# Kernel optimization log

Measured on AMD Instinct MI355X. Metric: run time of the kernel, lower is better.

## Reference

```python
import jax, jax.numpy as jnp
import numpy as np

B, E, T, H = 2, 1024, 2048, 16
DH = E // H


def _conv1x1(x, W, b, mask):
    # x: [B,C,T], W: [O,C], b: [O], mask: [B,1,T] (norm=False -> plain conv on masked input)
    x = x * mask
    return jnp.einsum('oc,bct->bot', W, x) + b[None, :, None]


def setup_inputs() -> dict:
    key = jax.random.key(0)
    ks = jax.random.split(key, 16)
    inp = {
        'q': jax.random.normal(ks[0], (B, E, T), jnp.float32),
        'k': jax.random.normal(ks[1], (B, E, T), jnp.float32),
        'v': jax.random.normal(ks[2], (B, E, T), jnp.float32),
        'query_mask': (jax.random.uniform(ks[3], (B, 1, T)) < 0.9).astype(jnp.float32),
        'key_mask': (jax.random.uniform(ks[4], (B, 1, T)) < 0.9).astype(jnp.float32),
        'value_mask': (jax.random.uniform(ks[5], (B, 1, T)) < 0.9).astype(jnp.float32),
        'Wq': jax.random.normal(ks[6], (E, E), jnp.float32) * (1.0 / np.sqrt(E)),
        'bq': jnp.zeros((E,), jnp.float32),
        'Wk': jax.random.normal(ks[7], (E, E), jnp.float32) * (1.0 / np.sqrt(E)),
        'bk': jnp.zeros((E,), jnp.float32),
        'Wv': jax.random.normal(ks[8], (E, E), jnp.float32) * (1.0 / np.sqrt(E)),
        'bv': jnp.zeros((E,), jnp.float32),
        'Wo': jax.random.normal(ks[9], (E, E), jnp.float32) * (1.0 / np.sqrt(E)),
        'bo': jnp.zeros((E,), jnp.float32),
    }
    return inp


def reference(q, k, v, query_mask, key_mask, value_mask, Wq, bq, Wk, bk, Wv, bv, Wo, bo):
    # 1x1 conv projections with input masking (norm=False path)
    qp = _conv1x1(q, Wq, bq, query_mask)   # [B,E,T]
    kp = _conv1x1(k, Wk, bk, key_mask)
    vp = _conv1x1(v, Wv, bv, value_mask)
    # split heads: [B,E,T] -> [B,H,DH,T]
    qh = qp.reshape(B, H, DH, T)
    kh = kp.reshape(B, H, DH, T)
    vh = vp.reshape(B, H, DH, T)
    # scores = q^T k with pre-softmax multiplicative masks, scaled by sqrt(embed_dim)
    scores = jnp.einsum('bhdq,bhdk->bhqk', qh, kh)
    scores = scores * query_mask[:, :, :, None] * key_mask[:, :, None, :] / np.sqrt(E)
    attn = jax.nn.softmax(scores, axis=-1) * key_mask[:, :, None, :]  # post-softmax mask
    # transpose_scores=False path: v @ scores (contracts v's time dim with the query dim)
    out = jnp.einsum('bhdq,bhqk->bhdk', vh, attn)  # [B,H,DH,T]
    out = out.reshape(B, E, T)
    return _conv1x1(out, Wo, bo, key_mask)
```

## Files before the change

### kernel.cpp

```cpp
#include <hip/hip_runtime.h>

#define B 2
#define E 1024
#define T 2048
#define H 16
#define DH 64

#define SCALE2 0.0450842200277801f

typedef _Float16 f16x8 __attribute__((ext_vector_type(8)));
typedef float f32x4 __attribute__((ext_vector_type(4)));
typedef float f32x16 __attribute__((ext_vector_type(16)));
typedef unsigned short ushort8v __attribute__((ext_vector_type(8)));
typedef unsigned int uint4v __attribute__((ext_vector_type(4)));

__device__ __forceinline__ f32x4 mfma16(f16x8 a, f16x8 b, f32x4 c) {
  return __builtin_amdgcn_mfma_f32_16x16x32_f16(a, b, c, 0, 0, 0);
}
__device__ __forceinline__ f32x16 mfma32(f16x8 a, f16x8 b, f32x16 c) {
  return __builtin_amdgcn_mfma_f32_32x32x16_f16(a, b, c, 0, 0, 0);
}
__device__ __forceinline__ unsigned short f16u(float x) {
  _Float16 h = (_Float16)x;
  return __builtin_bit_cast(unsigned short, h);
}
__device__ __forceinline__ float ex2(float x) {
  return __builtin_amdgcn_exp2f(x);
}
__device__ __forceinline__ unsigned int pk16(float a, float b) {
  auto h = __builtin_amdgcn_cvt_pkrtz(a, b);
  return __builtin_bit_cast(unsigned int, h);
}
__device__ __forceinline__ void plswap(unsigned int& a, unsigned int& b) {
  auto r = __builtin_amdgcn_permlane32_swap(a, b, false, false);
  a = r[0];
  b = r[1];
}

__global__ __launch_bounds__(256) void prep_weights(
    const float* __restrict__ Wq, const float* __restrict__ Wk,
    const float* __restrict__ Wv, const float* __restrict__ Wo,
    unsigned short* __restrict__ WqB, unsigned short* __restrict__ WkB,
    unsigned short* __restrict__ WvB, unsigned short* __restrict__ WoB) {
  const int which = blockIdx.y;
  const int i = (blockIdx.x * 256 + threadIdx.x) * 4;
  const float* src = which == 0 ? Wq : which == 1 ? Wk : which == 2 ? Wv : Wo;
  unsigned short* dst = which == 0 ? WqB : which == 1 ? WkB : which == 2 ? WvB : WoB;
  float4 v = *(const float4*)&src[i];
  ((unsigned int*)&dst[i])[0] = f16u(v.x) | ((unsigned)f16u(v.y) << 16);
  ((unsigned int*)&dst[i])[1] = f16u(v.z) | ((unsigned)f16u(v.w) << 16);
}

__global__ __launch_bounds__(256) void transpose_cvt(
    const float* __restrict__ q, const float* __restrict__ k,
    const float* __restrict__ v, unsigned short* __restrict__ XtQ,
    unsigned short* __restrict__ XtK, unsigned short* __restrict__ XtV) {
  __shared__ float Xs[32 * 36];
  const int z = blockIdx.z, which = z >> 1, b = z & 1;
  const float* X = which == 0 ? q : which == 1 ? k : v;
  unsigned short* O = which == 0 ? XtQ : which == 1 ? XtK : XtV;
  const int e0 = blockIdx.y * 32, t0 = blockIdx.x * 32;
  const int tid = threadIdx.x;
  const int r = tid >> 3, c = (tid & 7) * 4;
  *(float4*)&Xs[r * 36 + c] = *(const float4*)&X[((size_t)b * E + e0 + r) * T + t0 + c];
  __syncthreads();
  unsigned short h[4];
#pragma unroll
  for (int j = 0; j < 4; ++j) h[j] = f16u(Xs[(c + j) * 36 + r]);
  const size_t o = ((size_t)b * T + t0 + r) * E + e0 + c;
  ((unsigned int*)&O[o])[0] = h[0] | ((unsigned)h[1] << 16);
  ((unsigned int*)&O[o])[1] = h[2] | ((unsigned)h[3] << 16);
}

__global__ __launch_bounds__(256) void proj_qkv(
    const unsigned short* __restrict__ WqB, const unsigned short* __restrict__ WkB,
    const unsigned short* __restrict__ WvB, const unsigned short* __restrict__ XtQ,
    const unsigned short* __restrict__ XtK, const unsigned short* __restrict__ XtV,
    const float* __restrict__ bq, const float* __restrict__ bk,
    const float* __restrict__ bv, const float* __restrict__ qmask,
    const float* __restrict__ kmask, const float* __restrict__ vmask,
    unsigned short* __restrict__ qp2, unsigned short* __restrict__ kp2,
    unsigned short* __restrict__ vp) {
  __shared__ unsigned short Ah[128 * 72], Bs[128 * 72];
  const int b = blockIdx.z, my = blockIdx.y;
  const int which = my >> 3, o0 = (my & 7) * 128, t0 = blockIdx.x * 128;
  const unsigned short* W = which == 0 ? WqB : which == 1 ? WkB : WvB;
  const unsigned short* Xt = which == 0 ? XtQ : which == 1 ? XtK : XtV;
  const float* bias = which == 0 ? bq : which == 1 ? bk : bv;
  const float* mask = which == 0 ? qmask : which == 1 ? kmask : vmask;

  const int tid = threadIdx.x, wave = tid >> 6, lane = tid & 63;
  const int lg = lane & 15, quad = lane >> 4;
  const int wm = (wave & 1) * 64, wn = (wave >> 1) * 64;
  const int sr = tid >> 3, sc = (tid & 7) * 8;

  f32x4 acc[4][4];
#pragma unroll
  for (int i = 0; i < 4; ++i)
#pragma unroll
    for (int j = 0; j < 4; ++j) acc[i][j] = (f32x4){0.f, 0.f, 0.f, 0.f};

  for (int k0 = 0; k0 < E; k0 += 64) {
    ushort8v ra[4], rb[4];
#pragma unroll
    for (int p = 0; p < 4; ++p) {
      ra[p] = *(const ushort8v*)&W[(size_t)(o0 + p * 32 + sr) * E + k0 + sc];
      rb[p] = *(const ushort8v*)&Xt[((size_t)b * T + t0 + p * 32 + sr) * E + k0 + sc];
    }
    __syncthreads();
#pragma unroll
    for (int p = 0; p < 4; ++p) {
      *(ushort8v*)&Ah[(p * 32 + sr) * 72 + sc] = ra[p];
      *(ushort8v*)&Bs[(p * 32 + sr) * 72 + sc] = rb[p];
    }
    __syncthreads();
    f16x8 af[4][2];
#pragma unroll
    for (int mt = 0; mt < 4; ++mt) {
      af[mt][0] = *(const f16x8*)&Ah[(wm + mt * 16 + lg) * 72 + quad * 8];
      af[mt][1] = *(const f16x8*)&Ah[(wm + mt * 16 + lg) * 72 + 32 + quad * 8];
    }
#pragma unroll
    for (int nt = 0; nt < 4; ++nt) {
      f16x8 b0 = *(const f16x8*)&Bs[(wn + nt * 16 + lg) * 72 + quad * 8];
      f16x8 b1 = *(const f16x8*)&Bs[(wn + nt * 16 + lg) * 72 + 32 + quad * 8];
#pragma unroll
      for (int mt = 0; mt < 4; ++mt) {
        f32x4 c = acc[mt][nt];
        c = mfma16(af[mt][0], b0, c);
        c = mfma16(af[mt][1], b1, c);
        acc[mt][nt] = c;
      }
    }
  }
#pragma unroll
  for (int nt = 0; nt < 4; ++nt) {
    const int tcol = t0 + wn + nt * 16 + lg;
    const float mv = mask[b * T + tcol];
#pragma unroll
    for (int mt = 0; mt < 4; ++mt) {
      const int oF = o0 + wm + mt * 16 + quad * 4;
      float v4[4];
      if (which == 0) {
        const float s = mv * SCALE2;
#pragma unroll
        for (int r = 0; r < 4; ++r) v4[r] = (acc[mt][nt][r] + bias[oF + r]) * s;
      } else if (which == 1) {
#pragma unroll
        for (int r = 0; r < 4; ++r) v4[r] = (acc[mt][nt][r] + bias[oF + r]) * mv;
      } else {
#pragma unroll
        for (int r = 0; r < 4; ++r) v4[r] = acc[mt][nt][r] * mv + bias[oF + r];
      }
      if (which <= 1) {
        unsigned short* O = which == 0 ? qp2 : kp2;
        const int head = (o0 + wm) >> 6;
        const int bh2 = b * H + head;
        const size_t idx8 =
            (((size_t)(bh2 * (T / 32) + (tcol >> 5)) * 4 + mt) * 32 + (tcol & 31)) * 2 +
            (quad >> 1);
        unsigned int* dst = (unsigned int*)(O + idx8 * 8 + (quad & 1) * 4);
        dst[0] = f16u(v4[0]) | ((unsigned)f16u(v4[1]) << 16);
        dst[1] = f16u(v4[2]) | ((unsigned)f16u(v4[3]) << 16);
      } else {
#pragma unroll
        for (int r = 0; r < 4; ++r)
          vp[((size_t)b * E + oF + r) * T + tcol] = f16u(v4[r]);
      }
    }
  }
}

__global__ __launch_bounds__(256) void repack_v(
    const unsigned short* __restrict__ vp, unsigned short* __restrict__ vp2) {
  __shared__ unsigned short Ls[64 * 136];
  const int q0 = blockIdx.x * 128, hh = blockIdx.y, b = blockIdx.z;
  const int bh = b * H + hh;
  const int tid = threadIdx.x;
#pragma unroll
  for (int w = 0; w < 2; ++w) {
    const int d = w * 32 + (tid >> 3);
    const int c = (tid & 7) * 16;
    const unsigned short* src = vp + ((size_t)b * E + hh * DH + d) * T + q0 + c;
    *(ushort8v*)&Ls[d * 136 + c] = *(const ushort8v*)src;
    *(ushort8v*)&Ls[d * 136 + c + 8] = *(const ushort8v*)(src + 8);
  }
  __syncthreads();
#pragma unroll
  for (int w = 0; w < 4; ++w) {
    const int flat = w * 256 + tid;
    const int hb = flat & 1, lnv = (flat >> 1) & 31, dt = (flat >> 6) & 1,
              qgl = flat >> 7;
    ushort8v val = *(const ushort8v*)&Ls[(dt * 32 + lnv) * 136 + qgl * 16 + hb * 8];
    const size_t idx8 =
        (((size_t)(bh * (T / 16) + (q0 >> 4) + qgl) * 2 + dt) * 32 + lnv) * 2 + hb;
    *(ushort8v*)&vp2[idx8 * 8] = val;
  }
}

__global__ __launch_bounds__(256) void attn_stats(
    const unsigned short* __restrict__ qp2, const unsigned short* __restrict__ kp2,
    float* __restrict__ sPart) {
  const int bh = blockIdx.y;
  const int z = blockIdx.z;
  const int q0 = blockIdx.x * 128;
  const int tid = threadIdx.x, wave = tid >> 6, lane = tid & 63;
  const int ln = lane & 31, half = lane >> 5;

  const int t32q = (q0 >> 5) + wave;
  f16x8 aq[4];
#pragma unroll
  for (int s = 0; s < 4; ++s)
    aq[s] = *(const f16x8*)&qp2[((((size_t)bh * (T / 32) + t32q) * 4 + s) * 64 +
                                 ln * 2 + half) * 8];

  float lacc[16];
#pragma unroll
  for (int r = 0; r < 16; ++r) lacc[r] = 0.f;

  const int kbase = z * (T / 2);
  const int kend = kbase + T / 2;

  f16x8 bkr[2][4];
#pragma unroll
  for (int nt = 0; nt < 2; ++nt)
#pragma unroll
    for (int s = 0; s < 4; ++s)
      bkr[nt][s] = *(const f16x8*)&kp2[((((size_t)bh * (T / 32) + (kbase >> 5) + nt) * 4 +
                                         s) * 64 + ln * 2 + half) * 8];

  for (int kt = kbase; kt < kend; kt += 64) {
    const int kn = (kt + 64 < kend) ? kt + 64 : kbase;
    f16x8 nb[2][4];
#pragma unroll
    for (int nt = 0; nt < 2; ++nt)
#pragma unroll
      for (int s = 0; s < 4; ++s)
        nb[nt][s] =
            *(const f16x8*)&kp2[((((size_t)bh * (T / 32) + (kn >> 5) + nt) * 4 + s) * 64 +
                                 ln * 2 + half) * 8];
    f32x16 S0 = {}, S1 = {};
#pragma unroll
    for (int s = 0; s < 4; ++s) {
      S0 = mfma32(aq[s], bkr[0][s], S0);
      S1 = mfma32(aq[s], bkr[1][s], S1);
    }
#pragma unroll
    for (int r = 0; r < 16; ++r) lacc[r] += ex2(S0[r]) + ex2(S1[r]);
#pragma unroll
    for (int nt = 0; nt < 2; ++nt)
#pragma unroll
      for (int s = 0; s < 4; ++s) bkr[nt][s] = nb[nt][s];
  }
#pragma unroll
  for (int off = 1; off < 32; off <<= 1)
#pragma unroll
    for (int r = 0; r < 16; ++r) lacc[r] += __shfl_xor(lacc[r], off, 64);
  if (ln == 0) {
#pragma unroll
    for (int t = 0; t < 4; ++t) {
      f32x4 o;
#pragma unroll
      for (int j = 0; j < 4; ++j) o[j] = lacc[t * 4 + j];
      *(f32x4*)&sPart[((size_t)z * (B * H) + bh) * T + q0 + wave * 32 + t * 8 +
                      half * 4] = o;
    }
  }
}

__global__ __launch_bounds__(256) void stats_merge(
    const float* __restrict__ sPart, float* __restrict__ lLog) {
  const int i = (blockIdx.x * 256 + threadIdx.x) * 4;
  const int N = B * H * T;
  f32x4 a = *(const f32x4*)&sPart[i];
  f32x4 b = *(const f32x4*)&sPart[N + i];
  f32x4 o;
#pragma unroll
  for (int j = 0; j < 4; ++j) o[j] = -__builtin_amdgcn_logf(a[j] + b[j]);
  *(f32x4*)&lLog[i] = o;
}

__global__ __launch_bounds__(256) void attn_apply(
    const unsigned short* __restrict__ qp2, const unsigned short* __restrict__ kp2,
    const unsigned short* __restrict__ vp2, const float* __restrict__ lLog,
    float* __restrict__ aPart) {
  __shared__ float st[32 * 130];
  const int bh = blockIdx.y;
  const int z = blockIdx.z;
  const int kblk = blockIdx.x * 64;
  const int tid = threadIdx.x, wave = tid >> 6, lane = tid & 63;
  const int ln = lane & 31, half = lane >> 5;
  const int kt = wave & 1, qh = wave >> 1;

  const int t32k = (kblk >> 5) + kt;
  f16x8 bkk[4];
#pragma unroll
  for (int s = 0; s < 4; ++s)
    bkk[s] = *(const f16x8*)&kp2[((((size_t)bh * (T / 32) + t32k) * 4 + s) * 64 +
                                  ln * 2 + half) * 8];

  f32x16 acc0 = {}, acc1 = {};
  const int qstart = (z * 2 + qh) * (T / 4);
  const int qend = qstart + T / 4;

  f16x8 aqN[4], avN[2][2];
  f32x4 llN[4];
#pragma unroll
  for (int s = 0; s < 4; ++s)
    aqN[s] = *(const f16x8*)&qp2[((((size_t)bh * (T / 32) + (qstart >> 5)) * 4 + s) * 64 +
                                  ln * 2 + half) * 8];
#pragma unroll
  for (int dt = 0; dt < 2; ++dt)
#pragma unroll
    for (int f = 0; f < 2; ++f)
      avN[dt][f] = *(const f16x8*)&vp2[((((size_t)bh * (T / 16) + (qstart >> 4) + f) * 2 +
                                         dt) * 32 + ln) * 16 + half * 8];
#pragma unroll
  for (int t = 0; t < 4; ++t)
    llN[t] = *(const f32x4*)&lLog[(size_t)bh * T + qstart + t * 8 + half * 4];

  for (int qt = qstart; qt < qend; qt += 32) {
    f16x8 aq[4], av[2][2];
    f32x4 ll[4];
#pragma unroll
    for (int s = 0; s < 4; ++s) aq[s] = aqN[s];
#pragma unroll
    for (int dt = 0; dt < 2; ++dt)
#pragma unroll
      for (int f = 0; f < 2; ++f) av[dt][f] = avN[dt][f];
#pragma unroll
    for (int t = 0; t < 4; ++t) ll[t] = llN[t];
    const int qn = qt + 32 < qend ? qt + 32 : qstart;
#pragma unroll
    for (int s = 0; s < 4; ++s)
      aqN[s] = *(const f16x8*)&qp2[((((size_t)bh * (T / 32) + (qn >> 5)) * 4 + s) * 64 +
                                    ln * 2 + half) * 8];
#pragma unroll
    for (int dt = 0; dt < 2; ++dt)
#pragma unroll
      for (int f = 0; f < 2; ++f)
        avN[dt][f] = *(const f16x8*)&vp2[((((size_t)bh * (T / 16) + (qn >> 4) + f) * 2 +
                                           dt) * 32 + ln) * 16 + half * 8];
#pragma unroll
    for (int t = 0; t < 4; ++t)
      llN[t] = *(const f32x4*)&lLog[(size_t)bh * T + qn + t * 8 + half * 4];
    f32x16 S = {};
#pragma unroll
    for (int s = 0; s < 4; ++s) S = mfma32(aq[s], bkk[s], S);
    unsigned int w[8];
#pragma unroll
    for (int p = 0; p < 8; ++p) {
      const float e0 = ex2(S[p * 2 + 0] + ll[p >> 1][(p & 1) * 2 + 0]);
      const float e1 = ex2(S[p * 2 + 1] + ll[p >> 1][(p & 1) * 2 + 1]);
      w[p] = pk16(e0, e1);
    }
    plswap(w[0], w[2]);
    plswap(w[1], w[3]);
    plswap(w[4], w[6]);
    plswap(w[5], w[7]);
    uint4v f0, f1;
    f0[0] = w[0]; f0[1] = w[1]; f0[2] = w[2]; f0[3] = w[3];
    f1[0] = w[4]; f1[1] = w[5]; f1[2] = w[6]; f1[3] = w[7];
    const f16x8 pf0 = __builtin_bit_cast(f16x8, f0);
    const f16x8 pf1 = __builtin_bit_cast(f16x8, f1);
    acc0 = mfma32(av[0][0], pf0, acc0);
    acc0 = mfma32(av[0][1], pf1, acc0);
    acc1 = mfma32(av[1][0], pf0, acc1);
    acc1 = mfma32(av[1][1], pf1, acc1);
  }

  __syncthreads();
  if (qh == 1) {
#pragma unroll
    for (int i = 0; i < 16; ++i) {
      st[i * 130 + kt * 65 + lane] = acc0[i];
      st[(16 + i) * 130 + kt * 65 + lane] = acc1[i];
    }
  }
  __syncthreads();
  if (qh == 0) {
#pragma unroll
    for (int i = 0; i < 16; ++i) {
      acc0[i] += st[i * 130 + kt * 65 + lane];
      acc1[i] += st[(16 + i) * 130 + kt * 65 + lane];
    }
    const int kcol = kblk + kt * 32 + ln;
    float* dst = aPart + ((size_t)(z * B * H + bh) * T + kcol) * DH;
#pragma unroll
    for (int dt = 0; dt < 2; ++dt) {
      const float* a = dt ? (const float*)&acc1 : (const float*)&acc0;
#pragma unroll
      for (int t = 0; t < 4; ++t) {
        f32x4 o;
#pragma unroll
        for (int j = 0; j < 4; ++j) o[j] = a[t * 4 + j];
        *(f32x4*)&dst[dt * 32 + t * 8 + half * 4] = o;
      }
    }
  }
}

__global__ __launch_bounds__(256) void apply_merge(
    const float* __restrict__ aPart, unsigned short* __restrict__ ao) {
  const size_t i = ((size_t)blockIdx.x * 256 + threadIdx.x) * 8;
  const size_t NZ = (size_t)B * H * T * DH;
  f32x4 a0 = *(const f32x4*)&aPart[i];
  f32x4 a1 = *(const f32x4*)&aPart[i + 4];
  f32x4 b0 = *(const f32x4*)&aPart[NZ + i];
  f32x4 b1 = *(const f32x4*)&aPart[NZ + i + 4];
  unsigned short h[8];
#pragma unroll
  for (int j = 0; j < 4; ++j) h[j] = f16u(a0[j] + b0[j]);
#pragma unroll
  for (int j = 0; j < 4; ++j) h[4 + j] = f16u(a1[j] + b1[j]);
  const int bh = (int)(i >> 17);
  const int rem = (int)(i & (T * DH - 1));
  const int k = rem >> 6, d = rem & 63;
  uint4v u;
  u[0] = h[0] | ((unsigned)h[1] << 16);
  u[1] = h[2] | ((unsigned)h[3] << 16);
  u[2] = h[4] | ((unsigned)h[5] << 16);
  u[3] = h[6] | ((unsigned)h[7] << 16);
  *(uint4v*)&ao[((size_t)(bh >> 4) * T + k) * E + (bh & 15) * 64 + d] = u;
}

__global__ __launch_bounds__(256) void proj_final(
    const unsigned short* __restrict__ WoB, const unsigned short* __restrict__ ao,
    const float* __restrict__ bo, const float* __restrict__ kmask,
    float* __restrict__ out) {
  __shared__ unsigned short As[64 * 68], Bs[128 * 68];
  const int b = blockIdx.z, o0 = blockIdx.y * 64, t0 = blockIdx.x * 128;
  const int tid = threadIdx.x, wave = tid >> 6, lane = tid & 63;
  const int ln = lane & 31, half = lane >> 5;
  const int wn = wave * 32;
  const int ar = tid >> 2, ac = (tid & 3) * 16;
  const int br = tid >> 1, bc = (tid & 1) * 32;

  f32x16 acc0 = {}, acc1 = {};

  for (int k0 = 0; k0 < E; k0 += 64) {
    ushort8v a0 = *(const ushort8v*)&WoB[(size_t)(o0 + ar) * E + k0 + ac];
    ushort8v a1 = *(const ushort8v*)&WoB[(size_t)(o0 + ar) * E + k0 + ac + 8];
    ushort8v b0 = *(const ushort8v*)&ao[((size_t)b * T + t0 + br) * E + k0 + bc];
    ushort8v b1 = *(const ushort8v*)&ao[((size_t)b * T + t0 + br) * E + k0 + bc + 8];
    ushort8v b2 = *(const ushort8v*)&ao[((size_t)b * T + t0 + br) * E + k0 + bc + 16];
    ushort8v b3 = *(const ushort8v*)&ao[((size_t)b * T + t0 + br) * E + k0 + bc + 24];
    __syncthreads();
    *(ushort8v*)&As[ar * 68 + ac] = a0;
    *(ushort8v*)&As[ar * 68 + ac + 8] = a1;
    *(ushort8v*)&Bs[br * 68 + bc] = b0;
    *(ushort8v*)&Bs[br * 68 + bc + 8] = b1;
    *(ushort8v*)&Bs[br * 68 + bc + 16] = b2;
    *(ushort8v*)&Bs[br * 68 + bc + 24] = b3;
    __syncthreads();
#pragma unroll
    for (int s = 0; s < 4; ++s) {
      f16x8 af0 = *(const f16x8*)&As[ln * 68 + s * 16 + half * 8];
      f16x8 af1 = *(const f16x8*)&As[(32 + ln) * 68 + s * 16 + half * 8];
      f16x8 bf = *(const f16x8*)&Bs[(wn + ln) * 68 + s * 16 + half * 8];
      acc0 = mfma32(af0, bf, acc0);
      acc1 = mfma32(af1, bf, acc1);
    }
  }
  const int tcol = t0 + wn + ln;
  const float mv = kmask[b * T + tcol];
#pragma unroll
  for (int dt = 0; dt < 2; ++dt) {
    const float* a = dt ? (const float*)&acc1 : (const float*)&acc0;
#pragma unroll
    for (int t = 0; t < 4; ++t)
#pragma unroll
      for (int j = 0; j < 4; ++j) {
        const int e = o0 + dt * 32 + t * 8 + half * 4 + j;
        out[((size_t)b * E + e) * T + tcol] = a[t * 4 + j] * mv + bo[e];
      }
  }
}

extern "C" void kernel_launch(void* const* d_in, const int* in_sizes, int n_in,
                              void* d_out, int out_size, void* d_ws, size_t ws_size,
                              hipStream_t stream) {
  const float* q = (const float*)d_in[0];
  const float* k = (const float*)d_in[1];
  const float* v = (const float*)d_in[2];
  const float* qmask = (const float*)d_in[3];
  const float* kmask = (const float*)d_in[4];
  const float* vmask = (const float*)d_in[5];
  const float* Wq = (const float*)d_in[6];
  const float* bq = (const float*)d_in[7];
  const float* Wk = (const float*)d_in[8];
  const float* bk = (const float*)d_in[9];
  const float* Wv = (const float*)d_in[10];
  const float* bv = (const float*)d_in[11];
  const float* Wo = (const float*)d_in[12];
  const float* bo = (const float*)d_in[13];

  char* w = (char*)d_ws;
  const size_t WB = (size_t)E * E * sizeof(unsigned short);
  const size_t TB = (size_t)B * T * E * sizeof(unsigned short);
  unsigned short* WqB = (unsigned short*)(w + 0 * WB);
  unsigned short* WkB = (unsigned short*)(w + 1 * WB);
  unsigned short* WvB = (unsigned short*)(w + 2 * WB);
  unsigned short* WoB = (unsigned short*)(w + 3 * WB);
  size_t off = 4 * WB;
  unsigned short* XtQ = (unsigned short*)(w + off); off += TB;
  unsigned short* qp2 = (unsigned short*)(w + off); off += TB;
  unsigned short* kp2 = (unsigned short*)(w + off); off += TB;
  unsigned short* vp2 = (unsigned short*)(w + off); off += TB;
  float* lLog = (float*)(w + off); off += (size_t)B * H * T * sizeof(float);
  float* sPart = (float*)(w + off); off += (size_t)2 * B * H * T * sizeof(float);
  unsigned short* XtK = (unsigned short*)(w + off); off += TB;
  unsigned short* XtV = (unsigned short*)(w + off); off += TB;
  unsigned short* vp  = (unsigned short*)(w + off); off += TB;
  float* aPart = (float*)XtK;
  unsigned short* ao = XtQ;

  dim3 bl(256);
  prep_weights<<<dim3((E * E) / 1024, 4), bl, 0, stream>>>(
      Wq, Wk, Wv, Wo, WqB, WkB, WvB, WoB);
  transpose_cvt<<<dim3(T / 32, E / 32, 3 * B), bl, 0, stream>>>(
      q, k, v, XtQ, XtK, XtV);
  proj_qkv<<<dim3(T / 128, 24, B), bl, 0, stream>>>(
      WqB, WkB, WvB, XtQ, XtK, XtV, bq, bk, bv, qmask, kmask, vmask, qp2, kp2, vp);
  repack_v<<<dim3(T / 128, H, B), bl, 0, stream>>>(vp, vp2);
  attn_stats<<<dim3(T / 128, B * H, 2), bl, 0, stream>>>(qp2, kp2, sPart);
  stats_merge<<<dim3((B * H * T) / 1024), bl, 0, stream>>>(sPart, lLog);
  attn_apply<<<dim3(T / 64, B * H, 2), bl, 0, stream>>>(qp2, kp2, vp2, lLog, aPart);
  apply_merge<<<dim3((B * H * T * DH) / 2048), bl, 0, stream>>>(aPart, ao);
  proj_final<<<dim3(T / 128, E / 64, B), bl, 0, stream>>>(
      WoB, ao, bo, kmask, (float*)d_out);
}
```

Before: 282.1 us.

## Enlarge attention tiles, drop apply split-Q partials and fuse merge into attn_apply

attn_stats now gives each wave two 32-row query tiles, so every loaded K fragment is reused across twice as many queries. attn_apply covers 128 keys per block (64 per wave) over half the query range instead of splitting queries across grid z. This removes the fp32 aPart partial buffer and the apply_merge kernel, and the kernel writes fp16 output directly in the ao layout. The cost is more registers (four accumulators plus two score tiles), half as many blocks, and a longer serial loop per wave.

```diff
diff --git a/kernel.cpp b/kernel.cpp
--- a/kernel.cpp
+++ b/kernel.cpp
@@ -203,20 +203,22 @@
     float* __restrict__ sPart) {
   const int bh = blockIdx.y;
   const int z = blockIdx.z;
-  const int q0 = blockIdx.x * 128;
+  const int q0 = blockIdx.x * 256;
   const int tid = threadIdx.x, wave = tid >> 6, lane = tid & 63;
   const int ln = lane & 31, half = lane >> 5;
 
-  const int t32q = (q0 >> 5) + wave;
-  f16x8 aq[4];
-#pragma unroll
-  for (int s = 0; s < 4; ++s)
-    aq[s] = *(const f16x8*)&qp2[((((size_t)bh * (T / 32) + t32q) * 4 + s) * 64 +
-                                 ln * 2 + half) * 8];
-
-  float lacc[16];
-#pragma unroll
-  for (int r = 0; r < 16; ++r) lacc[r] = 0.f;
+  const int t32q = (q0 >> 5) + wave * 2;
+  f16x8 aq[2][4];
+#pragma unroll
+  for (int qs = 0; qs < 2; ++qs)
+#pragma unroll
+    for (int s = 0; s < 4; ++s)
+      aq[qs][s] = *(const f16x8*)&qp2[((((size_t)bh * (T / 32) + t32q + qs) * 4 + s) * 64 +
+                                       ln * 2 + half) * 8];
+
+  float lacc[32];
+#pragma unroll
+  for (int r = 0; r < 32; ++r) lacc[r] = 0.f;
 
   const int kbase = z * (T / 2);
   const int kend = kbase + T / 2;
@@ -239,14 +241,17 @@
         nb[nt][s] =
             *(const f16x8*)&kp2[((((size_t)bh * (T / 32) + (kn >> 5) + nt) * 4 + s) * 64 +
                                  ln * 2 + half) * 8];
-    f32x16 S0 = {}, S1 = {};
-#pragma unroll
-    for (int s = 0; s < 4; ++s) {
-      S0 = mfma32(aq[s], bkr[0][s], S0);
-      S1 = mfma32(aq[s], bkr[1][s], S1);
-    }
-#pragma unroll
-    for (int r = 0; r < 16; ++r) lacc[r] += ex2(S0[r]) + ex2(S1[r]);
+#pragma unroll
+    for (int qs = 0; qs < 2; ++qs) {
+      f32x16 S0 = {}, S1 = {};
+#pragma unroll
+      for (int s = 0; s < 4; ++s) {
+        S0 = mfma32(aq[qs][s], bkr[0][s], S0);
+        S1 = mfma32(aq[qs][s], bkr[1][s], S1);
+      }
+#pragma unroll
+      for (int r = 0; r < 16; ++r) lacc[qs * 16 + r] += ex2(S0[r]) + ex2(S1[r]);
+    }
 #pragma unroll
     for (int nt = 0; nt < 2; ++nt)
 #pragma unroll
@@ -255,16 +260,18 @@
 #pragma unroll
   for (int off = 1; off < 32; off <<= 1)
 #pragma unroll
-    for (int r = 0; r < 16; ++r) lacc[r] += __shfl_xor(lacc[r], off, 64);
+    for (int r = 0; r < 32; ++r) lacc[r] += __shfl_xor(lacc[r], off, 64);
   if (ln == 0) {
 #pragma unroll
-    for (int t = 0; t < 4; ++t) {
-      f32x4 o;
-#pragma unroll
-      for (int j = 0; j < 4; ++j) o[j] = lacc[t * 4 + j];
-      *(f32x4*)&sPart[((size_t)z * (B * H) + bh) * T + q0 + wave * 32 + t * 8 +
-                      half * 4] = o;
-    }
+    for (int qs = 0; qs < 2; ++qs)
+#pragma unroll
+      for (int t = 0; t < 4; ++t) {
+        f32x4 o;
+#pragma unroll
+        for (int j = 0; j < 4; ++j) o[j] = lacc[qs * 16 + t * 4 + j];
+        *(f32x4*)&sPart[((size_t)z * (B * H) + bh) * T + q0 + wave * 64 + qs * 32 +
+                        t * 8 + half * 4] = o;
+      }
   }
 }
 
@@ -283,28 +290,28 @@
 __global__ __launch_bounds__(256) void attn_apply(
     const unsigned short* __restrict__ qp2, const unsigned short* __restrict__ kp2,
     const unsigned short* __restrict__ vp2, const float* __restrict__ lLog,
-    float* __restrict__ aPart) {
-  __shared__ float st[32 * 130];
-  const int bh = blockIdx.y;
-  const int z = blockIdx.z;
-  const int kblk = blockIdx.x * 64;
+    unsigned short* __restrict__ ao) {
+  __shared__ float st[64 * 130];
+  const int bh = blockIdx.y, b = bh >> 4, h = bh & 15;
+  const int kblk = blockIdx.x * 128;
   const int tid = threadIdx.x, wave = tid >> 6, lane = tid & 63;
   const int ln = lane & 31, half = lane >> 5;
   const int kt = wave & 1, qh = wave >> 1;
 
-  const int t32k = (kblk >> 5) + kt;
-  f16x8 bkk[4];
-#pragma unroll
-  for (int s = 0; s < 4; ++s)
-    bkk[s] = *(const f16x8*)&kp2[((((size_t)bh * (T / 32) + t32k) * 4 + s) * 64 +
-                                  ln * 2 + half) * 8];
-
-  f32x16 acc0 = {}, acc1 = {};
-  const int qstart = (z * 2 + qh) * (T / 4);
-  const int qend = qstart + T / 4;
+  const int t32k = (kblk >> 5) + kt * 2;
+  f16x8 bkk[2][4];
+#pragma unroll
+  for (int sub = 0; sub < 2; ++sub)
+#pragma unroll
+    for (int s = 0; s < 4; ++s)
+      bkk[sub][s] = *(const f16x8*)&kp2[((((size_t)bh * (T / 32) + t32k + sub) * 4 + s) *
+                                             64 + ln * 2 + half) * 8];
+
+  f32x16 acc00 = {}, acc01 = {}, acc10 = {}, acc11 = {};
+  const int qstart = qh * (T / 2);
+  const int qend = qstart + T / 2;
 
   f16x8 aqN[4], avN[2][2];
-  f32x4 llN[4];
 #pragma unroll
   for (int s = 0; s < 4; ++s)
     aqN[s] = *(const f16x8*)&qp2[((((size_t)bh * (T / 32) + (qstart >> 5)) * 4 + s) * 64 +
@@ -315,21 +322,15 @@
     for (int f = 0; f < 2; ++f)
       avN[dt][f] = *(const f16x8*)&vp2[((((size_t)bh * (T / 16) + (qstart >> 4) + f) * 2 +
                                          dt) * 32 + ln) * 16 + half * 8];
-#pragma unroll
-  for (int t = 0; t < 4; ++t)
-    llN[t] = *(const f32x4*)&lLog[(size_t)bh * T + qstart + t * 8 + half * 4];
 
   for (int qt = qstart; qt < qend; qt += 32) {
     f16x8 aq[4], av[2][2];
-    f32x4 ll[4];
 #pragma unroll
     for (int s = 0; s < 4; ++s) aq[s] = aqN[s];
 #pragma unroll
     for (int dt = 0; dt < 2; ++dt)
 #pragma unroll
       for (int f = 0; f < 2; ++f) av[dt][f] = avN[dt][f];
-#pragma unroll
-    for (int t = 0; t < 4; ++t) ll[t] = llN[t];
     const int qn = qt + 32 < qend ? qt + 32 : qstart;
 #pragma unroll
     for (int s = 0; s < 4; ++s)
@@ -341,87 +342,98 @@
       for (int f = 0; f < 2; ++f)
         avN[dt][f] = *(const f16x8*)&vp2[((((size_t)bh * (T / 16) + (qn >> 4) + f) * 2 +
                                            dt) * 32 + ln) * 16 + half * 8];
+    f32x4 ll[4];
 #pragma unroll
     for (int t = 0; t < 4; ++t)
-      llN[t] = *(const f32x4*)&lLog[(size_t)bh * T + qn + t * 8 + half * 4];
-    f32x16 S = {};
-#pragma unroll
-    for (int s = 0; s < 4; ++s) S = mfma32(aq[s], bkk[s], S);
-    unsigned int w[8];
-#pragma unroll
-    for (int p = 0; p < 8; ++p) {
-      const float e0 = ex2(S[p * 2 + 0] + ll[p >> 1][(p & 1) * 2 + 0]);
-      const float e1 = ex2(S[p * 2 + 1] + ll[p >> 1][(p & 1) * 2 + 1]);
-      w[p] = pk16(e0, e1);
-    }
-    plswap(w[0], w[2]);
-    plswap(w[1], w[3]);
-    plswap(w[4], w[6]);
-    plswap(w[5], w[7]);
-    uint4v f0, f1;
-    f0[0] = w[0]; f0[1] = w[1]; f0[2] = w[2]; f0[3] = w[3];
-    f1[0] = w[4]; f1[1] = w[5]; f1[2] = w[6]; f1[3] = w[7];
-    const f16x8 pf0 = __builtin_bit_cast(f16x8, f0);
-    const f16x8 pf1 = __builtin_bit_cast(f16x8, f1);
-    acc0 = mfma32(av[0][0], pf0, acc0);
-    acc0 = mfma32(av[0][1], pf1, acc0);
-    acc1 = mfma32(av[1][0], pf0, acc1);
-    acc1 = mfma32(av[1][1], pf1, acc1);
+      ll[t] = *(const f32x4*)&lLog[(size_t)bh * T + qt + t * 8 + half * 4];
+    f32x16 S0 = {}, S1 = {};
+#pragma unroll
+    for (int s = 0; s < 4; ++s) S0 = mfma32(aq[s], bkk[0][s], S0);
+#pragma unroll
+    for (int s = 0; s < 4; ++s) S1 = mfma32(aq[s], bkk[1][s], S1);
+    {
+      unsigned int w[8];
+#pragma unroll
+      for (int p = 0; p < 8; ++p) {
+        const float e0 = ex2(S0[p * 2 + 0] + ll[p >> 1][(p & 1) * 2 + 0]);
+        const float e1 = ex2(S0[p * 2 + 1] + ll[p >> 1][(p & 1) * 2 + 1]);
+        w[p] = pk16(e0, e1);
+      }
+      plswap(w[0], w[2]);
+      plswap(w[1], w[3]);
+      plswap(w[4], w[6]);
+      plswap(w[5], w[7]);
+      uint4v f0v, f1v;
+      f0v[0] = w[0]; f0v[1] = w[1]; f0v[2] = w[2]; f0v[3] = w[3];
+      f1v[0] = w[4]; f1v[1] = w[5]; f1v[2] = w[6]; f1v[3] = w[7];
+      const f16x8 pf0 = __builtin_bit_cast(f16x8, f0v);
+      const f16x8 pf1 = __builtin_bit_cast(f16x8, f1v);
+      acc00 = mfma32(av[0][0], pf0, acc00);
+      acc00 = mfma32(av[0][1], pf1, acc00);
+      acc01 = mfma32(av[1][0], pf0, acc01);
+      acc01 = mfma32(av[1][1], pf1, acc01);
+    }
+    {
+      unsigned int w[8];
+#pragma unroll
+      for (int p = 0; p < 8; ++p) {
+        const float e0 = ex2(S1[p * 2 + 0] + ll[p >> 1][(p & 1) * 2 + 0]);
+        const float e1 = ex2(S1[p * 2 + 1] + ll[p >> 1][(p & 1) * 2 + 1]);
+        w[p] = pk16(e0, e1);
+      }
+      plswap(w[0], w[2]);
+      plswap(w[1], w[3]);
+      plswap(w[4], w[6]);
+      plswap(w[5], w[7]);
+      uint4v f0v, f1v;
+      f0v[0] = w[0]; f0v[1] = w[1]; f0v[2] = w[2]; f0v[3] = w[3];
+      f1v[0] = w[4]; f1v[1] = w[5]; f1v[2] = w[6]; f1v[3] = w[7];
+      const f16x8 pf0 = __builtin_bit_cast(f16x8, f0v);
+      const f16x8 pf1 = __builtin_bit_cast(f16x8, f1v);
+      acc10 = mfma32(av[0][0], pf0, acc10);
+      acc10 = mfma32(av[0][1], pf1, acc10);
+      acc11 = mfma32(av[1][0], pf0, acc11);
+      acc11 = mfma32(av[1][1], pf1, acc11);
+    }
   }
 
   __syncthreads();
   if (qh == 1) {
 #pragma unroll
     for (int i = 0; i < 16; ++i) {
-      st[i * 130 + kt * 65 + lane] = acc0[i];
-      st[(16 + i) * 130 + kt * 65 + lane] = acc1[i];
+      st[(0 * 16 + i) * 130 + kt * 65 + lane] = acc00[i];
+      st[(1 * 16 + i) * 130 + kt * 65 + lane] = acc01[i];
+      st[(2 * 16 + i) * 130 + kt * 65 + lane] = acc10[i];
+      st[(3 * 16 + i) * 130 + kt * 65 + lane] = acc11[i];
     }
   }
   __syncthreads();
   if (qh == 0) {
 #pragma unroll
     for (int i = 0; i < 16; ++i) {
-      acc0[i] += st[i * 130 + kt * 65 + lane];
-      acc1[i] += st[(16 + i) * 130 + kt * 65 + lane];
-    }
-    const int kcol = kblk + kt * 32 + ln;
-    float* dst = aPart + ((size_t)(z * B * H + bh) * T + kcol) * DH;
-#pragma unroll
-    for (int dt = 0; dt < 2; ++dt) {
-      const float* a = dt ? (const float*)&acc1 : (const float*)&acc0;
-#pragma unroll
-      for (int t = 0; t < 4; ++t) {
-        f32x4 o;
-#pragma unroll
-        for (int j = 0; j < 4; ++j) o[j] = a[t * 4 + j];
-        *(f32x4*)&dst[dt * 32 + t * 8 + half * 4] = o;
-      }
-    }
-  }
-}
-
-__global__ __launch_bounds__(256) void apply_merge(
-    const float* __restrict__ aPart, unsigned short* __restrict__ ao) {
-  const size_t i = ((size_t)blockIdx.x * 256 + threadIdx.x) * 8;
-  const size_t NZ = (size_t)B * H * T * DH;
-  f32x4 a0 = *(const f32x4*)&aPart[i];
-  f32x4 a1 = *(const f32x4*)&aPart[i + 4];
-  f32x4 b0 = *(const f32x4*)&aPart[NZ + i];
-  f32x4 b1 = *(const f32x4*)&aPart[NZ + i + 4];
-  unsigned short h[8];
-#pragma unroll
-  for (int j = 0; j < 4; ++j) h[j] = f16u(a0[j] + b0[j]);
-#pragma unroll
-  for (int j = 0; j < 4; ++j) h[4 + j] = f16u(a1[j] + b1[j]);
-  const int bh = (int)(i >> 17);
-  const int rem = (int)(i & (T * DH - 1));
-  const int k = rem >> 6, d = rem & 63;
-  uint4v u;
-  u[0] = h[0] | ((unsigned)h[1] << 16);
-  u[1] = h[2] | ((unsigned)h[3] << 16);
-  u[2] = h[4] | ((unsigned)h[5] << 16);
-  u[3] = h[6] | ((unsigned)h[7] << 16);
-  *(uint4v*)&ao[((size_t)(bh >> 4) * T + k) * E + (bh & 15) * 64 + d] = u;
+      acc00[i] += st[(0 * 16 + i) * 130 + kt * 65 + lane];
+      acc01[i] += st[(1 * 16 + i) * 130 + kt * 65 + lane];
+      acc10[i] += st[(2 * 16 + i) * 130 + kt * 65 + lane];
+      acc11[i] += st[(3 * 16 + i) * 130 + kt * 65 + lane];
+    }
+#pragma unroll
+    for (int sub = 0; sub < 2; ++sub) {
+      const int kcol = kblk + kt * 64 + sub * 32 + ln;
+      const size_t obase = ((size_t)b * T + kcol) * E + h * DH;
+#pragma unroll
+      for (int dt = 0; dt < 2; ++dt) {
+        const float* a = sub == 0 ? (dt ? (const float*)&acc01 : (const float*)&acc00)
+                                  : (dt ? (const float*)&acc11 : (const float*)&acc10);
+#pragma unroll
+        for (int t = 0; t < 4; ++t) {
+          uint2 wv;
+          wv.x = f16u(a[t * 4 + 0]) | ((unsigned)f16u(a[t * 4 + 1]) << 16);
+          wv.y = f16u(a[t * 4 + 2]) | ((unsigned)f16u(a[t * 4 + 3]) << 16);
+          *(uint2*)&ao[obase + dt * 32 + t * 8 + half * 4] = wv;
+        }
+      }
+    }
+  }
 }
 
 __global__ __launch_bounds__(256) void proj_final(
@@ -512,7 +524,6 @@
   unsigned short* XtK = (unsigned short*)(w + off); off += TB;
   unsigned short* XtV = (unsigned short*)(w + off); off += TB;
   unsigned short* vp  = (unsigned short*)(w + off); off += TB;
-  float* aPart = (float*)XtK;
   unsigned short* ao = XtQ;
 
   dim3 bl(256);
@@ -523,10 +534,9 @@
   proj_qkv<<<dim3(T / 128, 24, B), bl, 0, stream>>>(
       WqB, WkB, WvB, XtQ, XtK, XtV, bq, bk, bv, qmask, kmask, vmask, qp2, kp2, vp);
   repack_v<<<dim3(T / 128, H, B), bl, 0, stream>>>(vp, vp2);
-  attn_stats<<<dim3(T / 128, B * H, 2), bl, 0, stream>>>(qp2, kp2, sPart);
+  attn_stats<<<dim3(T / 256, B * H, 2), bl, 0, stream>>>(qp2, kp2, sPart);
   stats_merge<<<dim3((B * H * T) / 1024), bl, 0, stream>>>(sPart, lLog);
-  attn_apply<<<dim3(T / 64, B * H, 2), bl, 0, stream>>>(qp2, kp2, vp2, lLog, aPart);
-  apply_merge<<<dim3((B * H * T * DH) / 2048), bl, 0, stream>>>(aPart, ao);
+  attn_apply<<<dim3(T / 128, B * H), bl, 0, stream>>>(qp2, kp2, vp2, lLog, ao);
   proj_final<<<dim3(T / 128, E / 64, B), bl, 0, stream>>>(
       WoB, ao, bo, kmask, (float*)d_out);
 }
```

After: 276.8 us. No clear change (-1.9%).
